# Performance work log

Measured on AMD Instinct MI355X. Metric: run time of the kernel, lower is better.

Reference implementation:

```python
import jax, jax.numpy as jnp
import numpy as np

N_LAYERS = 4
D_IN = 64
D_OUT = 64
D_MODEL = 512
D_STATE = 256
RMIN, RMAX, MAX_PHASE = 0.8, 0.95, 2.0 * np.pi


def setup_inputs() -> dict:
    key = jax.random.key(0)
    rng = np.random.default_rng(0)
    B, L = 8, 2048
    u = jax.random.normal(key, (B, L, D_IN), dtype=jnp.float32)
    # encoder/decoder (nn.Linear, bias=False): weight shape [out, in]
    encoder_w = jnp.asarray(rng.standard_normal((D_MODEL, D_IN)) / np.sqrt(D_IN), jnp.float32)
    decoder_w = jnp.asarray(rng.standard_normal((D_OUT, D_MODEL)) / np.sqrt(D_MODEL), jnp.float32)
    # LRU params per block (standard ring init on eigenvalues)
    u1 = rng.uniform(size=(N_LAYERS, D_STATE))
    u2 = rng.uniform(size=(N_LAYERS, D_STATE))
    nu_log = jnp.asarray(np.log(-0.5 * np.log(u1 * (RMAX**2 - RMIN**2) + RMIN**2)), jnp.float32)
    theta_log = jnp.asarray(np.log(MAX_PHASE * u2), jnp.float32)
    B_re = jnp.asarray(rng.standard_normal((N_LAYERS, D_STATE, D_MODEL)) / np.sqrt(2 * D_MODEL), jnp.float32)
    B_im = jnp.asarray(rng.standard_normal((N_LAYERS, D_STATE, D_MODEL)) / np.sqrt(2 * D_MODEL), jnp.float32)
    C_re = jnp.asarray(rng.standard_normal((N_LAYERS, D_MODEL, D_STATE)) / np.sqrt(D_STATE), jnp.float32)
    C_im = jnp.asarray(rng.standard_normal((N_LAYERS, D_MODEL, D_STATE)) / np.sqrt(D_STATE), jnp.float32)
    D = jnp.asarray(rng.standard_normal((N_LAYERS, D_MODEL)), jnp.float32)
    # GLU feedforward: y = (x W1^T) * sigmoid(x W2^T)
    W1 = jnp.asarray(rng.standard_normal((N_LAYERS, D_MODEL, D_MODEL)) / np.sqrt(D_MODEL), jnp.float32)
    W2 = jnp.asarray(rng.standard_normal((N_LAYERS, D_MODEL, D_MODEL)) / np.sqrt(D_MODEL), jnp.float32)
    res_logit = jnp.full((N_LAYERS,), -1.0, jnp.float32)
    return dict(u=u, encoder_w=encoder_w, decoder_w=decoder_w, nu_log=nu_log,
                theta_log=theta_log, B_re=B_re, B_im=B_im, C_re=C_re, C_im=C_im,
                D=D, W1=W1, W2=W2, res_logit=res_logit)


def _lru(x, nu, th, Bre, Bim, Cre, Cim, Dv):
    # diagonal complex LRU: h_t = lam*h_{t-1} + gamma*B u_t ; y = Re(C h) + D*u
    lam = jnp.exp(-jnp.exp(nu) + 1j * jnp.exp(th)).astype(jnp.complex64)  # [N]
    gam = jnp.sqrt(1.0 - jnp.abs(lam) ** 2).astype(jnp.complex64)
    Bc = (Bre + 1j * Bim).astype(jnp.complex64)  # [N, D]
    Bu = jnp.einsum('bld,nd->bln', x.astype(jnp.complex64), Bc) * gam  # [B,L,N]
    lam_b = jnp.broadcast_to(lam, Bu.shape)

    def comb(a, b):
        return (a[0] * b[0], a[1] * b[0] + b[1])

    _, h = jax.lax.associative_scan(comb, (lam_b, Bu), axis=1)
    Cc = (Cre + 1j * Cim).astype(jnp.complex64)  # [D, N]
    return jnp.real(jnp.einsum('bln,dn->bld', h, Cc)) + Dv * x


def reference(u, encoder_w, decoder_w, nu_log, theta_log, B_re, B_im, C_re, C_im, D, W1, W2, res_logit):
    x = jnp.einsum('bli,mi->blm', u, encoder_w)  # encoder
    for k in range(N_LAYERS):
        z = _lru(x, nu_log[k], theta_log[k], B_re[k], B_im[k], C_re[k], C_im[k], D[k])
        z = jnp.einsum('bld,od->blo', z, W1[k]) * jax.nn.sigmoid(jnp.einsum('bld,od->blo', z, W2[k]))
        x = x + jax.nn.sigmoid(res_logit[k]) * z  # gated residual (dropout=0)
    return jnp.einsum('blm,om->blo', x, decoder_w)  # decoder
```

## Files before the change

kernel.cpp:

```cpp
#include <hip/hip_runtime.h>
#include <cmath>

#define DM 512
#define DS 256
#define NL 4
#define BATCH 8
#define SEQ 2048
#define MROWS (BATCH*SEQ)
#define LCH 32
#define NCH 64

typedef unsigned short ushort_t;
typedef unsigned int uint_t;
typedef __attribute__((ext_vector_type(8))) short short8;
typedef __attribute__((ext_vector_type(4))) float floatx4;

__device__ __forceinline__ float sigmoidf_(float v) { return 1.0f / (1.0f + __expf(-v)); }

__device__ __forceinline__ ushort_t f2bf(float f) {
    union { float f; unsigned int u; } c; c.f = f;
    unsigned int u = c.u;
    u += 0x7fffu + ((u >> 16) & 1u);
    return (ushort_t)(u >> 16);
}
__device__ __forceinline__ float bf2f(uint_t h) {
    union { unsigned int u; float f; } c; c.u = (h & 0xffffu) << 16; return c.f;
}
__device__ __forceinline__ uint_t pack2(float a, float b) {
    return (uint_t)f2bf(a) | ((uint_t)f2bf(b) << 16);
}

#define AS1 __attribute__((address_space(1)))
#define AS3 __attribute__((address_space(3)))
__device__ __forceinline__ void gl_lds16(const void* g, void* l) {
    __builtin_amdgcn_global_load_lds((const AS1 uint_t*)g, (AS3 uint_t*)l, 16, 0, 0);
}

struct GemmArgs {
    const ushort_t* A;
    const ushort_t* Wa;
    const ushort_t* Wb;
    const ushort_t* xbf_in;
    const float* gam;
    const float* Dv;
    float* of32;
    ushort_t* obf;
    const float* resp;
    const float* lamre;
    const float* lamim;
    float* carry;
    int K;
    int N;
    int layer;
};

#define PREFETCH_TILE(it_, buf_)                                                        \
    do {                                                                                \
        const size_t kb_ = (size_t)(it_) * 64;                                          \
        char* dst_ = smem + (buf_) * HALF;                                              \
        gl_lds16(Ap + (size_t)(wid * 16 + lrow) * Kb + kb_, dst_ + wid * 1024);         \
        gl_lds16(Ap + (size_t)((wid + 4) * 16 + lrow) * Kb + kb_,                       \
                 dst_ + (wid + 4) * 1024);                                              \
        gl_lds16(B0p + (size_t)(wid * 16 + lrow) * Kb + kb_, dst_ + AB + wid * 1024);   \
        if constexpr (BN == 128) {                                                      \
            gl_lds16(B0p + (size_t)((wid + 4) * 16 + lrow) * Kb + kb_,                  \
                     dst_ + AB + (wid + 4) * 1024);                                     \
        }                                                                               \
        if constexpr (DUAL) {                                                           \
            gl_lds16(B1p + (size_t)(wid * 16 + lrow) * Kb + kb_,                        \
                     dst_ + AB + BB + wid * 1024);                                      \
            if constexpr (BN == 128) {                                                  \
                gl_lds16(B1p + (size_t)((wid + 4) * 16 + lrow) * Kb + kb_,              \
                         dst_ + AB + BB + (wid + 4) * 1024);                            \
            }                                                                           \
        }                                                                               \
    } while (0)

template<int BN, int EPI, int DUAL>
__launch_bounds__(256, DUAL ? 2 : 3)
__global__ void mgemm(const GemmArgs p) {
    constexpr int BM = 128;
    constexpr int MT = (BN == 128) ? 4 : 2;
    constexpr int NT = 4;
    constexpr int WROWS = MT * 16;
    constexpr int AB = 8192;
    constexpr int BB = (BN == 128) ? 8192 : 4096;
    constexpr int B1B = DUAL ? BB : 0;
    constexpr int HALF = AB + BB + B1B;
    constexpr int EPB = (EPI == 4) ? 0 : 64 * 132 * 4;
    constexpr int SMB = (2 * HALF > EPB) ? 2 * HALF : EPB;
    __shared__ __align__(16) char smem[SMB];

    const int K = p.K, N = p.N;
    const int tid = threadIdx.x, lane = tid & 63, wid = tid >> 6;
    const int wm = (BN == 128) ? (wid & 1) : wid;
    const int wn = (BN == 128) ? (wid >> 1) : 0;
    const int m0 = blockIdx.x * BM, n0 = blockIdx.y * BN;
    const int q = lane >> 4, r16 = lane & 15;
    const int lrow = lane >> 2;
    const size_t Kb = (size_t)K * 2;
    const char* Ap  = (const char*)p.A  + (size_t)m0 * Kb + (lane & 3) * 16;
    const char* B0p = (const char*)p.Wa + (size_t)n0 * Kb + (lane & 3) * 16;
    const char* B1p = (const char*)p.Wb + (size_t)n0 * Kb + (lane & 3) * 16;

    floatx4 acc0[MT][NT] = {};
    floatx4 acc1[DUAL ? MT : 1][DUAL ? NT : 1] = {};

    const int iters = K >> 5;
    PREFETCH_TILE(0, 0);
    for (int it = 0; it < iters; ++it) {
        __syncthreads();
        if (it + 1 < iters) PREFETCH_TILE(it + 1, (it + 1) & 1);
        const ushort_t* As  = (const ushort_t*)(smem + (it & 1) * HALF);
        const ushort_t* Bs0 = (const ushort_t*)(smem + (it & 1) * HALF + AB);
        const ushort_t* Bs1 = (const ushort_t*)(smem + (it & 1) * HALF + AB + BB);

        short8 af[MT], b0[NT], b1[DUAL ? NT : 1];
#pragma unroll
        for (int i = 0; i < MT; ++i)
            af[i] = *(const short8*)&As[(wm * WROWS + i * 16 + r16) * 32 + q * 8];
#pragma unroll
        for (int j = 0; j < NT; ++j) {
            b0[j] = *(const short8*)&Bs0[(wn * 64 + j * 16 + r16) * 32 + q * 8];
            if constexpr (DUAL)
                b1[j] = *(const short8*)&Bs1[(wn * 64 + j * 16 + r16) * 32 + q * 8];
        }
#pragma unroll
        for (int i = 0; i < MT; ++i)
#pragma unroll
            for (int j = 0; j < NT; ++j) {
                acc0[i][j] = __builtin_amdgcn_mfma_f32_16x16x32_bf16(af[i], b0[j], acc0[i][j], 0, 0, 0);
                if constexpr (DUAL)
                    acc1[i][j] = __builtin_amdgcn_mfma_f32_16x16x32_bf16(af[i], b1[j], acc1[i][j], 0, 0, 0);
            }
    }

    if constexpr (EPI == 4) {
#pragma unroll
        for (int i = 0; i < MT; ++i)
#pragma unroll
            for (int j = 0; j < NT; ++j)
#pragma unroll
                for (int rr = 0; rr < 4; ++rr) {
                    const int row = m0 + wm * WROWS + i * 16 + q * 4 + rr;
                    const int col = wn * 64 + j * 16 + r16;
                    p.of32[(size_t)row * N + col] = acc0[i][j][rr];
                }
        return;
    } else {
        float* eps = (float*)smem;
        float rsv = 0.f;
        if constexpr (EPI == 3) rsv = sigmoidf_(p.resp[p.layer]);
        constexpr int ERND = 2;

#pragma unroll
        for (int i = 0; i < MT; i += ERND) {
            __syncthreads();
#pragma unroll
            for (int ii = 0; ii < ERND; ++ii) {
#pragma unroll
                for (int j = 0; j < NT; ++j) {
                    const int colt = wn * 64 + j * 16 + r16;
#pragma unroll
                    for (int rr = 0; rr < 4; ++rr) {
                        float v = acc0[i + ii][j][rr];
                        if constexpr (EPI == 3) v = rsv * v * sigmoidf_(acc1[i + ii][j][rr]);
                        eps[(ii * 32 + wm * 16 + q * 4 + rr) * 132 + colt] = v;
                    }
                }
            }
            __syncthreads();
            const int row_r = tid >> 3, colg = (tid & 7) * 16;
#pragma unroll
            for (int ii = 0; ii < ERND; ++ii) {
                const int lr = (row_r >> 4) * 64 + (i + ii) * 16 + (row_r & 15);
                const int grow = m0 + lr;
                const int gcol = n0 + colg;
                float4 f[4];
#pragma unroll
                for (int c = 0; c < 4; ++c)
                    f[c] = *(float4*)&eps[(ii * 32 + row_r) * 132 + colg + c * 4];
                const size_t ob = (size_t)grow * N + gcol;

                if constexpr (EPI == 3) {
                    uint_t xp[8];
                    *(uint4*)(xp)     = *(const uint4*)(p.xbf_in + ob);
                    *(uint4*)(xp + 4) = *(const uint4*)(p.xbf_in + ob + 8);
#pragma unroll
                    for (int c = 0; c < 4; ++c) {
                        f[c].x += bf2f(xp[2 * c]);
                        f[c].y += bf2f(xp[2 * c] >> 16);
                        f[c].z += bf2f(xp[2 * c + 1]);
                        f[c].w += bf2f(xp[2 * c + 1] >> 16);
                    }
                }
                uint4 p0, p1;
                p0.x = pack2(f[0].x, f[0].y); p0.y = pack2(f[0].z, f[0].w);
                p0.z = pack2(f[1].x, f[1].y); p0.w = pack2(f[1].z, f[1].w);
                p1.x = pack2(f[2].x, f[2].y); p1.y = pack2(f[2].z, f[2].w);
                p1.z = pack2(f[3].x, f[3].y); p1.w = pack2(f[3].z, f[3].w);
                *(uint4*)(p.obf + ob) = p0;
                *(uint4*)(p.obf + ob + 8) = p1;
            }
        }
    }
}

template<int EPI>
__launch_bounds__(256, 3)
__global__ void sgemm64(const GemmArgs p) {
    constexpr int BM = 128;
    constexpr int MT = 4, NT = 4;
    constexpr int AB = 16384;
    constexpr int BB = 16384;
    constexpr int HALF = AB + BB;
    constexpr int EPB = (EPI == 1) ? (32 * 132 * 4 + 128 * 66 * 4) : 64 * 132 * 4;
    constexpr int SMB = (2 * HALF > EPB) ? 2 * HALF : EPB;
    __shared__ __align__(16) char smem[SMB];

    const int K = p.K, N = p.N;
    const int tid = threadIdx.x, lane = tid & 63, wid = tid >> 6;
    const int wm = wid & 1, wn = wid >> 1;
    const int m0 = blockIdx.x * BM, n0 = blockIdx.y * 128;
    const int q = lane >> 4, r16 = lane & 15;
    const int lrow = lane >> 2;
    const size_t Kb = (size_t)K * 2;
    const char* Ap  = (const char*)p.A  + (size_t)m0 * Kb + (lane & 3) * 16;
    const char* B0p = (const char*)p.Wa + (size_t)n0 * Kb + (lane & 3) * 16;

    floatx4 acc0[MT][NT] = {};

#define PFS(it_, buf_)                                                                      \
    do {                                                                                    \
        const size_t kb0_ = (size_t)(it_) * 128;                                            \
        {                                                                       \
            const size_t kb_ = kb0_;                                                        \
            char* dst_ = smem + (buf_) * HALF;                                              \
            gl_lds16(Ap + (size_t)(wid * 16 + lrow) * Kb + kb_, dst_ + wid * 1024);         \
            gl_lds16(Ap + (size_t)((wid + 4) * 16 + lrow) * Kb + kb_,                       \
                     dst_ + (wid + 4) * 1024);                                              \
            gl_lds16(B0p + (size_t)(wid * 16 + lrow) * Kb + kb_, dst_ + AB + wid * 1024);   \
            gl_lds16(B0p + (size_t)((wid + 4) * 16 + lrow) * Kb + kb_,                      \
                     dst_ + AB + (wid + 4) * 1024);                                         \
        }                                                                                   \
        {                                                                       \
            const size_t kb_ = kb0_ + 64;                                                   \
            char* dst_ = smem + (buf_) * HALF + 8192;                                       \
            gl_lds16(Ap + (size_t)(wid * 16 + lrow) * Kb + kb_, dst_ + wid * 1024);         \
            gl_lds16(Ap + (size_t)((wid + 4) * 16 + lrow) * Kb + kb_,                       \
                     dst_ + (wid + 4) * 1024);                                              \
            gl_lds16(B0p + (size_t)(wid * 16 + lrow) * Kb + kb_, dst_ + AB + wid * 1024);   \
            gl_lds16(B0p + (size_t)((wid + 4) * 16 + lrow) * Kb + kb_,                      \
                     dst_ + AB + (wid + 4) * 1024);                                         \
        }                                                                                   \
    } while (0)

    const int iters = K >> 6;
    PFS(0, 0);
    for (int it = 0; it < iters; ++it) {
        __syncthreads();
        if (it + 1 < iters) PFS(it + 1, (it + 1) & 1);
        const ushort_t* As  = (const ushort_t*)(smem + (it & 1) * HALF);
        const ushort_t* Bs0 = (const ushort_t*)(smem + (it & 1) * HALF + AB);

#pragma unroll
        for (int ks = 0; ks < 2; ++ks) {
            short8 af[MT], b0[NT];
#pragma unroll
            for (int i = 0; i < MT; ++i)
                af[i] = *(const short8*)&As[ks * 4096 + (wm * 64 + i * 16 + r16) * 32 + q * 8];
#pragma unroll
            for (int j = 0; j < NT; ++j)
                b0[j] = *(const short8*)&Bs0[ks * 4096 + (wn * 64 + j * 16 + r16) * 32 + q * 8];
#pragma unroll
            for (int i = 0; i < MT; ++i)
#pragma unroll
                for (int j = 0; j < NT; ++j)
                    acc0[i][j] = __builtin_amdgcn_mfma_f32_16x16x32_bf16(af[i], b0[j], acc0[i][j], 0, 0, 0);
        }
    }
#undef PFS

    float* eps = (float*)smem;
    uint_t* zst = (uint_t*)(smem + 32 * 132 * 4);
    constexpr int ERND = (EPI == 1) ? 1 : 2;

#pragma unroll
    for (int i = 0; i < MT; i += ERND) {
        __syncthreads();
#pragma unroll
        for (int ii = 0; ii < ERND; ++ii) {
#pragma unroll
            for (int j = 0; j < NT; ++j) {
                const int colt = wn * 64 + j * 16 + r16;
#pragma unroll
                for (int rr = 0; rr < 4; ++rr) {
                    float v = acc0[i + ii][j][rr];
                    if constexpr (EPI == 1) v *= p.gam[(n0 + colt) >> 1];
                    eps[(ii * 32 + wm * 16 + q * 4 + rr) * 132 + colt] = v;
                }
            }
        }
        __syncthreads();
        const int row_r = tid >> 3, colg = (tid & 7) * 16;
#pragma unroll
        for (int ii = 0; ii < ERND; ++ii) {
            const int lr = (row_r >> 4) * 64 + (i + ii) * 16 + (row_r & 15);
            const int grow = m0 + lr;
            const int gcol = n0 + colg;
            float4 f[4];
#pragma unroll
            for (int c = 0; c < 4; ++c)
                f[c] = *(float4*)&eps[(ii * 32 + row_r) * 132 + colg + c * 4];
            const size_t ob = (size_t)grow * N + gcol;

            if constexpr (EPI == 2) {
                uint_t xp[8];
                *(uint4*)(xp)     = *(const uint4*)(p.xbf_in + ob);
                *(uint4*)(xp + 4) = *(const uint4*)(p.xbf_in + ob + 8);
#pragma unroll
                for (int c = 0; c < 4; ++c) {
                    float4 dv = *(const float4*)(p.Dv + gcol + c * 4);
                    f[c].x += dv.x * bf2f(xp[2 * c]);
                    f[c].y += dv.y * bf2f(xp[2 * c] >> 16);
                    f[c].z += dv.z * bf2f(xp[2 * c + 1]);
                    f[c].w += dv.w * bf2f(xp[2 * c + 1] >> 16);
                }
            }
            uint4 p0, p1;
            p0.x = pack2(f[0].x, f[0].y); p0.y = pack2(f[0].z, f[0].w);
            p0.z = pack2(f[1].x, f[1].y); p0.w = pack2(f[1].z, f[1].w);
            p1.x = pack2(f[2].x, f[2].y); p1.y = pack2(f[2].z, f[2].w);
            p1.z = pack2(f[3].x, f[3].y); p1.w = pack2(f[3].z, f[3].w);
            *(uint4*)(p.obf + ob) = p0;
            *(uint4*)(p.obf + ob + 8) = p1;
            if constexpr (EPI == 1) {
                const int c0 = colg >> 1;
                *(uint4*)&zst[lr * 66 + c0]     = p0;
                *(uint4*)&zst[lr * 66 + c0 + 4] = p1;
            }
        }
    }

    if constexpr (EPI == 1) {
        __syncthreads();
        const int c4 = tid >> 6, s6 = tid & 63;
        const int sg = (n0 >> 1) + s6;
        const float lr_ = p.lamre[sg], li_ = p.lamim[sg];
        float hr = 0.f, hi = 0.f;
#pragma unroll 8
        for (int i2 = 0; i2 < LCH; ++i2) {
            uint_t uu = zst[(c4 * LCH + i2) * 66 + s6];
            float br = bf2f(uu), bi = bf2f(uu >> 16);
            float nr = fmaf(lr_, hr, fmaf(-li_, hi, br));
            float ni = fmaf(lr_, hi, fmaf(li_, hr, bi));
            hr = nr; hi = ni;
        }
        const int b = m0 >> 11;
        const int cblk = ((m0 & (SEQ - 1)) >> 5) + c4;
        const size_t cb = (size_t)(b * NCH + cblk) * 512 + sg;
        p.carry[cb] = hr; p.carry[cb + DS] = hi;
    }
}

__global__ void prep_all(const float* __restrict__ u, const float* __restrict__ enc,
                         const float* __restrict__ dec, const float* __restrict__ nu,
                         const float* __restrict__ th,
                         const float* __restrict__ Bre, const float* __restrict__ Bim,
                         const float* __restrict__ Cre, const float* __restrict__ Cim,
                         const float* __restrict__ W1, const float* __restrict__ W2,
                         ushort_t* __restrict__ WBb, ushort_t* __restrict__ Wzb,
                         ushort_t* __restrict__ W1b, ushort_t* __restrict__ W2b,
                         ushort_t* __restrict__ encb, ushort_t* __restrict__ decb,
                         ushort_t* __restrict__ ubf,
                         float* __restrict__ lre, float* __restrict__ lim,
                         float* __restrict__ gm) {
    const int idx = blockIdx.x * 256 + threadIdx.x;
    const int k = idx & 511, n = (idx >> 9) & 511, l = idx >> 18;
    {
        const int s = n >> 1, part = n & 1;
        const float* src = part ? Bim : Bre;
        WBb[idx] = f2bf(src[((size_t)l * DS + s) * DM + k]);
    }
    {
        const int s = k >> 1, part = k & 1;
        float v = part ? -Cim[((size_t)l * DM + n) * DS + s]
                       :  Cre[((size_t)l * DM + n) * DS + s];
        Wzb[idx] = f2bf(v);
    }
    W1b[idx] = f2bf(W1[idx]);
    W2b[idx] = f2bf(W2[idx]);
    ubf[idx] = f2bf(u[idx]);
    if (idx < DM * 64) { encb[idx] = f2bf(enc[idx]); decb[idx] = f2bf(dec[idx]); }
    if (idx < NL * DS) {
        float a = expf(-expf(nu[idx])), t = expf(th[idx]);
        lre[idx] = a * cosf(t);
        lim[idx] = a * sinf(t);
        gm[idx] = sqrtf(fmaxf(0.f, 1.f - a * a));
    }
}

__global__ __launch_bounds__(256) void scan_apply_lb(
        const uint_t* __restrict__ Bu, const float* __restrict__ lre_,
        const float* __restrict__ lim_, const float* __restrict__ carry,
        uint_t* __restrict__ h) {
    const int s = threadIdx.x;
    const int blk = blockIdx.x, b = blk >> 6, c = blk & 63;
    const float lre = lre_[s], lim = lim_[s];

    float gre = 0.f, gim = 0.f;
    if (c > 0) {
        float are = lre, aim = lim;
#pragma unroll
        for (int t = 0; t < 5; ++t) {
            float nr = are * are - aim * aim, ni = 2.f * are * aim;
            are = nr; aim = ni;
        }
        const int depth = (c < 12) ? c : 12;
        float pwr = 1.f, pwi = 0.f;
        for (int j = c - 1; j >= c - depth; --j) {
            const size_t jb = (size_t)(b * NCH + j) * 512 + s;
            float er = carry[jb], ei = carry[jb + DS];
            gre = fmaf(pwr, er, fmaf(-pwi, ei, gre));
            gim = fmaf(pwr, ei, fmaf(pwi, er, gim));
            float nr = pwr * are - pwi * aim, ni = pwr * aim + pwi * are;
            pwr = nr; pwi = ni;
        }
    }

    float hr = gre, hi = gim;
    size_t base = ((size_t)b * SEQ + (size_t)c * LCH) * DS + s;
#pragma unroll 8
    for (int i = 0; i < LCH; ++i, base += DS) {
        uint_t uu = Bu[base];
        float br = bf2f(uu), bi = bf2f(uu >> 16);
        float nr = fmaf(lre, hr, fmaf(-lim, hi, br));
        float ni = fmaf(lre, hi, fmaf(lim, hr, bi));
        hr = nr; hi = ni;
        h[base] = pack2(hr, hi);
    }
}

extern "C" void kernel_launch(void* const* d_in, const int* in_sizes, int n_in,
                              void* d_out, int out_size, void* d_ws, size_t ws_size,
                              hipStream_t stream) {
    const float* u   = (const float*)d_in[0];
    const float* enc = (const float*)d_in[1];
    const float* dec = (const float*)d_in[2];
    const float* nu  = (const float*)d_in[3];
    const float* th  = (const float*)d_in[4];
    const float* Bre = (const float*)d_in[5];
    const float* Bim = (const float*)d_in[6];
    const float* Cre = (const float*)d_in[7];
    const float* Cim = (const float*)d_in[8];
    const float* Dp  = (const float*)d_in[9];
    const float* W1  = (const float*)d_in[10];
    const float* W2  = (const float*)d_in[11];
    const float* res = (const float*)d_in[12];
    float* out = (float*)d_out;

    const size_t MD = (size_t)MROWS * DM;
    float* carry = (float*)d_ws;
    float* lre  = carry + (size_t)BATCH * NCH * 512;
    float* lim  = lre + NL * DS;
    float* gmt  = lim + NL * DS;
    ushort_t* xbf  = (ushort_t*)(gmt + NL * DS);
    ushort_t* Bubf = xbf + MD;
    ushort_t* hbf  = Bubf + MD;
    ushort_t* zbf  = hbf + MD;
    ushort_t* ubf  = zbf;
    ushort_t* WBb  = zbf + MD;
    ushort_t* Wzb  = WBb + (size_t)NL * DM * DM;
    ushort_t* W1b  = Wzb + (size_t)NL * DM * DM;
    ushort_t* W2b  = W1b + (size_t)NL * DM * DM;
    ushort_t* encb = W2b + (size_t)NL * DM * DM;
    ushort_t* decb = encb + DM * 64;

    prep_all<<<NL * DM * DM / 256, 256, 0, stream>>>(
        u, enc, dec, nu, th, Bre, Bim, Cre, Cim, W1, W2,
        WBb, Wzb, W1b, W2b, encb, decb, ubf, lre, lim, gmt);

    const dim3 gFull(MROWS / 128, DM / 128);

    {
        GemmArgs a = {};
        a.A = ubf; a.Wa = encb; a.K = 64; a.N = DM;
        a.obf = xbf;
        sgemm64<0><<<gFull, 256, 0, stream>>>(a);
    }

    for (int k = 0; k < NL; ++k) {
        {
            GemmArgs a = {};
            a.A = xbf; a.Wa = WBb + (size_t)k * DM * DM; a.K = DM; a.N = DM;
            a.obf = Bubf; a.gam = gmt + k * DS;
            a.lamre = lre + k * DS; a.lamim = lim + k * DS; a.carry = carry;
            sgemm64<1><<<gFull, 256, 0, stream>>>(a);
        }
        scan_apply_lb<<<BATCH * NCH, 256, 0, stream>>>((const uint_t*)Bubf,
                                                       lre + k * DS, lim + k * DS, carry,
                                                       (uint_t*)hbf);
        {
            GemmArgs a = {};
            a.A = hbf; a.Wa = Wzb + (size_t)k * DM * DM; a.K = DM; a.N = DM;
            a.obf = zbf; a.xbf_in = xbf; a.Dv = Dp + k * DM;
            sgemm64<2><<<gFull, 256, 0, stream>>>(a);
        }
        {
            GemmArgs a = {};
            a.A = zbf; a.Wa = W1b + (size_t)k * DM * DM; a.Wb = W2b + (size_t)k * DM * DM;
            a.K = DM; a.N = DM;
            a.obf = xbf; a.xbf_in = xbf; a.resp = res; a.layer = k;
            mgemm<128, 3, 1><<<gFull, 256, 0, stream>>>(a);
        }
    }
    {
        GemmArgs a = {};
        a.A = xbf; a.Wa = decb; a.K = DM; a.N = 64;
        a.of32 = out;
        mgemm<64, 4, 0><<<dim3(MROWS / 128, 1), 256, 0, stream>>>(a);
    }
}
```

Before: 378.5 us.

## Triple-buffer sgemm K-loop with 32-wide stages and partial vmcnt waits

```diff
diff --git a/kernel.cpp b/kernel.cpp
--- a/kernel.cpp
+++ b/kernel.cpp
@@ -208,14 +208,13 @@
 
 template<int EPI>
 __launch_bounds__(256, 3)
-__global__ void sgemm64(const GemmArgs p) {
+__global__ void sgemm_p(const GemmArgs p) {
     constexpr int BM = 128;
     constexpr int MT = 4, NT = 4;
-    constexpr int AB = 16384;
-    constexpr int BB = 16384;
+    constexpr int AB = 8192, BB = 8192;
     constexpr int HALF = AB + BB;
     constexpr int EPB = (EPI == 1) ? (32 * 132 * 4 + 128 * 66 * 4) : 64 * 132 * 4;
-    constexpr int SMB = (2 * HALF > EPB) ? 2 * HALF : EPB;
+    constexpr int SMB = (3 * HALF > EPB) ? 3 * HALF : EPB;
     __shared__ __align__(16) char smem[SMB];
 
     const int K = p.K, N = p.N;
@@ -230,56 +229,47 @@
 
     floatx4 acc0[MT][NT] = {};
 
-#define PFS(it_, buf_)                                                                      \
-    do {                                                                                    \
-        const size_t kb0_ = (size_t)(it_) * 128;                                            \
-        {                                                                       \
-            const size_t kb_ = kb0_;                                                        \
-            char* dst_ = smem + (buf_) * HALF;                                              \
-            gl_lds16(Ap + (size_t)(wid * 16 + lrow) * Kb + kb_, dst_ + wid * 1024);         \
-            gl_lds16(Ap + (size_t)((wid + 4) * 16 + lrow) * Kb + kb_,                       \
-                     dst_ + (wid + 4) * 1024);                                              \
-            gl_lds16(B0p + (size_t)(wid * 16 + lrow) * Kb + kb_, dst_ + AB + wid * 1024);   \
-            gl_lds16(B0p + (size_t)((wid + 4) * 16 + lrow) * Kb + kb_,                      \
-                     dst_ + AB + (wid + 4) * 1024);                                         \
-        }                                                                                   \
-        {                                                                       \
-            const size_t kb_ = kb0_ + 64;                                                   \
-            char* dst_ = smem + (buf_) * HALF + 8192;                                       \
-            gl_lds16(Ap + (size_t)(wid * 16 + lrow) * Kb + kb_, dst_ + wid * 1024);         \
-            gl_lds16(Ap + (size_t)((wid + 4) * 16 + lrow) * Kb + kb_,                       \
-                     dst_ + (wid + 4) * 1024);                                              \
-            gl_lds16(B0p + (size_t)(wid * 16 + lrow) * Kb + kb_, dst_ + AB + wid * 1024);   \
-            gl_lds16(B0p + (size_t)((wid + 4) * 16 + lrow) * Kb + kb_,                      \
-                     dst_ + AB + (wid + 4) * 1024);                                         \
-        }                                                                                   \
+#define PFP(it_, buf_)                                                                  \
+    do {                                                                                \
+        const size_t kb_ = (size_t)(it_) * 64;                                          \
+        char* dst_ = smem + (buf_) * HALF;                                              \
+        gl_lds16(Ap + (size_t)(wid * 16 + lrow) * Kb + kb_, dst_ + wid * 1024);         \
+        gl_lds16(Ap + (size_t)((wid + 4) * 16 + lrow) * Kb + kb_,                       \
+                 dst_ + (wid + 4) * 1024);                                              \
+        gl_lds16(B0p + (size_t)(wid * 16 + lrow) * Kb + kb_, dst_ + AB + wid * 1024);   \
+        gl_lds16(B0p + (size_t)((wid + 4) * 16 + lrow) * Kb + kb_,                      \
+                 dst_ + AB + (wid + 4) * 1024);                                         \
     } while (0)
 
-    const int iters = K >> 6;
-    PFS(0, 0);
+    const int iters = K >> 5;
+    PFP(0, 0);
+    if (iters > 1) PFP(1, 1);
+    int b0i = 0, b2i = 2;
     for (int it = 0; it < iters; ++it) {
-        __syncthreads();
-        if (it + 1 < iters) PFS(it + 1, (it + 1) & 1);
-        const ushort_t* As  = (const ushort_t*)(smem + (it & 1) * HALF);
-        const ushort_t* Bs0 = (const ushort_t*)(smem + (it & 1) * HALF + AB);
-
-#pragma unroll
-        for (int ks = 0; ks < 2; ++ks) {
-            short8 af[MT], b0[NT];
-#pragma unroll
-            for (int i = 0; i < MT; ++i)
-                af[i] = *(const short8*)&As[ks * 4096 + (wm * 64 + i * 16 + r16) * 32 + q * 8];
+        if (it + 1 < iters) asm volatile("s_waitcnt vmcnt(4)" ::: "memory");
+        else                asm volatile("s_waitcnt vmcnt(0)" ::: "memory");
+        __builtin_amdgcn_s_barrier();
+        if (it + 2 < iters) PFP(it + 2, b2i);
+        const ushort_t* As  = (const ushort_t*)(smem + b0i * HALF);
+        const ushort_t* Bs0 = (const ushort_t*)(smem + b0i * HALF + AB);
+
+        short8 af[MT], b0[NT];
+#pragma unroll
+        for (int i = 0; i < MT; ++i)
+            af[i] = *(const short8*)&As[(wm * 64 + i * 16 + r16) * 32 + q * 8];
+#pragma unroll
+        for (int j = 0; j < NT; ++j)
+            b0[j] = *(const short8*)&Bs0[(wn * 64 + j * 16 + r16) * 32 + q * 8];
+#pragma unroll
+        for (int i = 0; i < MT; ++i)
 #pragma unroll
             for (int j = 0; j < NT; ++j)
-                b0[j] = *(const short8*)&Bs0[ks * 4096 + (wn * 64 + j * 16 + r16) * 32 + q * 8];
-#pragma unroll
-            for (int i = 0; i < MT; ++i)
-#pragma unroll
-                for (int j = 0; j < NT; ++j)
-                    acc0[i][j] = __builtin_amdgcn_mfma_f32_16x16x32_bf16(af[i], b0[j], acc0[i][j], 0, 0, 0);
-        }
-    }
-#undef PFS
+                acc0[i][j] = __builtin_amdgcn_mfma_f32_16x16x32_bf16(af[i], b0[j], acc0[i][j], 0, 0, 0);
+
+        b0i = (b0i == 2) ? 0 : b0i + 1;
+        b2i = (b2i == 2) ? 0 : b2i + 1;
+    }
+#undef PFP
 
     float* eps = (float*)smem;
     uint_t* zst = (uint_t*)(smem + 32 * 132 * 4);
@@ -486,7 +476,7 @@
         GemmArgs a = {};
         a.A = ubf; a.Wa = encb; a.K = 64; a.N = DM;
         a.obf = xbf;
-        sgemm64<0><<<gFull, 256, 0, stream>>>(a);
+        sgemm_p<0><<<gFull, 256, 0, stream>>>(a);
     }
 
     for (int k = 0; k < NL; ++k) {
@@ -495,7 +485,7 @@
             a.A = xbf; a.Wa = WBb + (size_t)k * DM * DM; a.K = DM; a.N = DM;
             a.obf = Bubf; a.gam = gmt + k * DS;
             a.lamre = lre + k * DS; a.lamim = lim + k * DS; a.carry = carry;
-            sgemm64<1><<<gFull, 256, 0, stream>>>(a);
+            sgemm_p<1><<<gFull, 256, 0, stream>>>(a);
         }
         scan_apply_lb<<<BATCH * NCH, 256, 0, stream>>>((const uint_t*)Bubf,
                                                        lre + k * DS, lim + k * DS, carry,
@@ -504,7 +494,7 @@
             GemmArgs a = {};
             a.A = hbf; a.Wa = Wzb + (size_t)k * DM * DM; a.K = DM; a.N = DM;
             a.obf = zbf; a.xbf_in = xbf; a.Dv = Dp + k * DM;
-            sgemm64<2><<<gFull, 256, 0, stream>>>(a);
+            sgemm_p<2><<<gFull, 256, 0, stream>>>(a);
         }
         {
             GemmArgs a = {};
```

Measured after the change: 369.4 us. 1.02x faster.
